# Performance work log

Hardware: AMD Instinct MI355X
Metric: run time of the kernel (lower is better)

The kernel has to match this reference:

```python
import jax, jax.numpy as jnp
import numpy as np

N_NODES = 50000
N_EDGES = 800000
NUM_GRAPHS = 256
BN_EPS = 1e-5


def setup_inputs() -> dict:
    key = jax.random.key(0)
    ks = jax.random.split(key, 16)
    in_dim, hid, out_dim = 64, 128, 1
    s = lambda k, shape, fan: jax.random.normal(k, shape, jnp.float32) / np.sqrt(fan)
    inp = {
        'x': jax.random.normal(ks[0], (N_NODES, in_dim), jnp.float32),
        'edge_index': jax.random.randint(ks[1], (2, N_EDGES), 0, N_NODES, jnp.int64),
        'batch': jnp.sort(jax.random.randint(ks[2], (N_NODES,), 0, NUM_GRAPHS, jnp.int64)),
        # SAGEConv layer 0 (in_dim->hid): Wn aggregated-neighbor weight (with bias), Wr root weight
        'Wn0': s(ks[3], (in_dim, hid), in_dim), 'Wr0': s(ks[4], (in_dim, hid), in_dim), 'b0': jnp.zeros((hid,), jnp.float32),
        'Wn1': s(ks[5], (hid, hid), hid), 'Wr1': s(ks[6], (hid, hid), hid), 'b1': jnp.zeros((hid,), jnp.float32),
        'Wn2': s(ks[7], (hid, hid), hid), 'Wr2': s(ks[8], (hid, hid), hid), 'b2': jnp.zeros((hid,), jnp.float32),
        'gamma': jnp.ones((3, hid), jnp.float32), 'beta': jnp.zeros((3, hid), jnp.float32),
        'fc1_W': s(ks[9], (hid, hid // 2), hid), 'fc1_b': jnp.zeros((hid // 2,), jnp.float32),
        'fc2_W': s(ks[10], (hid // 2, out_dim), hid // 2), 'fc2_b': jnp.zeros((out_dim,), jnp.float32),
    }
    return inp


def _sage_mean(x, src, dst, inv_deg, Wn, Wr, b):
    # mean-aggregate neighbor features then linear: lin_l(mean_j x_j) + lin_r(x_i)
    agg = jax.ops.segment_sum(x[src], dst, num_segments=N_NODES) * inv_deg
    return agg @ Wn + x @ Wr + b


def _bn_relu(h, g, bta):
    mu = jnp.mean(h, axis=0)
    var = jnp.var(h, axis=0)
    return jax.nn.relu((h - mu) * jax.lax.rsqrt(var + BN_EPS) * g + bta)


def reference(x, edge_index, batch, Wn0, Wr0, b0, Wn1, Wr1, b1, Wn2, Wr2, b2,
              gamma, beta, fc1_W, fc1_b, fc2_W, fc2_b):
    src, dst = edge_index[0], edge_index[1]
    deg = jax.ops.segment_sum(jnp.ones((src.shape[0],), x.dtype), dst, num_segments=N_NODES)
    inv_deg = (1.0 / jnp.maximum(deg, 1.0))[:, None]  # [N,1]

    h = _bn_relu(_sage_mean(x, src, dst, inv_deg, Wn0, Wr0, b0), gamma[0], beta[0])
    h = _bn_relu(_sage_mean(h, src, dst, inv_deg, Wn1, Wr1, b1), gamma[1], beta[1])
    h = _bn_relu(_sage_mean(h, src, dst, inv_deg, Wn2, Wr2, b2), gamma[2], beta[2])

    # global mean pool over graphs
    pooled = jax.ops.segment_sum(h, batch, num_segments=NUM_GRAPHS)
    cnt = jax.ops.segment_sum(jnp.ones((h.shape[0],), h.dtype), batch, num_segments=NUM_GRAPHS)
    pooled = pooled / jnp.maximum(cnt, 1.0)[:, None]

    z = jax.nn.relu(pooled @ fc1_W + fc1_b)
    return jax.nn.sigmoid(z @ fc2_W + fc2_b)  # [NUM_GRAPHS, 1]
```

## Files before the change

kernel.cpp:

```cpp
#include <hip/hip_runtime.h>

#define N_NODES 50000
#define N_EDGES 800000
#define NUM_GRAPHS 256
#define HID 128
#define IN_DIM 64
#define BN_EPS 1e-5f
#define SPREAD 16
#define NB 196
#define BUCKET 256
#define SCHUNK 4096
#define NCHUNK 196
#define PX_BLKS 1563
#define W0_BLKS 8
#define W1_BLKS 16

typedef __attribute__((ext_vector_type(8))) short bf16x8;
typedef __attribute__((ext_vector_type(4))) float f32x4;

__device__ __forceinline__ float bf2f(unsigned short u){ union{unsigned i;float f;}c; c.i=((unsigned)u)<<16; return c.f; }
__device__ __forceinline__ float bflo(unsigned w){ union{unsigned i;float f;}c; c.i=w<<16; return c.f; }
__device__ __forceinline__ float bfhi(unsigned w){ union{unsigned i;float f;}c; c.i=w&0xFFFF0000u; return c.f; }
__device__ __forceinline__ unsigned short f2bf(float f){ union{float f;unsigned i;}c; c.f=f; unsigned r=c.i+0x7FFF+((c.i>>16)&1); return (unsigned short)(r>>16); }
__device__ __forceinline__ unsigned fpack(float a, float b){
  union{float f;unsigned i;}ca,cb; ca.f=a; cb.f=b;
  unsigned ra=((ca.i+0x7FFF+((ca.i>>16)&1))>>16)&0xFFFFu;
  unsigned rb=(cb.i+0x7FFF+((cb.i>>16)&1))&0xFFFF0000u;
  return ra|rb;
}
__device__ __forceinline__ void acc8(float* a, uint4 u){
  a[0]+=bflo(u.x); a[1]+=bfhi(u.x); a[2]+=bflo(u.y); a[3]+=bfhi(u.y);
  a[4]+=bflo(u.z); a[5]+=bfhi(u.z); a[6]+=bflo(u.w); a[7]+=bfhi(u.w);
}

__global__ __launch_bounds__(256) void k_hist(const int* __restrict__ dst, int* __restrict__ bcount){
  __shared__ int h[NB];
  int t = threadIdx.x;
  for(int i=t;i<NB;i+=256) h[i]=0;
  __syncthreads();
  int base = blockIdx.x*SCHUNK;
  int n = min(SCHUNK, N_EDGES-base);
  for(int v=t; v<n; v+=256) atomicAdd(&h[dst[base+v]>>8], 1);
  __syncthreads();
  for(int i=t;i<NB;i+=256) if(h[i]) atomicAdd(&bcount[i], h[i]);
}

__global__ __launch_bounds__(256) void k_scatter_pack(const int* __restrict__ src, const int* __restrict__ dst,
      const int* __restrict__ bcount, int* __restrict__ bfill, unsigned* __restrict__ pairs,
      const float* __restrict__ x, unsigned short* __restrict__ H0,
      const float* __restrict__ Wn0, const float* __restrict__ Wr0, unsigned short* __restrict__ Bp0,
      const float* __restrict__ Wn1, const float* __restrict__ Wr1, unsigned short* __restrict__ Bp1,
      const float* __restrict__ Wn2, const float* __restrict__ Wr2, unsigned short* __restrict__ Bp2){
  __shared__ int h[NB], lbase[NB], gbase[NB], cur[NB];
  __shared__ int sc[256];
  __shared__ unsigned staged[SCHUNK];
  int blk = blockIdx.x, t = threadIdx.x;
  if(blk < NCHUNK){
    for(int i=t;i<NB;i+=256) h[i]=0;
    __syncthreads();
    int base = blk*SCHUNK;
    int n = min(SCHUNK, N_EDGES-base);
    for(int v=t; v<n; v+=256) atomicAdd(&h[dst[base+v]>>8], 1);
    __syncthreads();
    int bc = (t<NB)? bcount[t] : 0;
    sc[t]=bc; __syncthreads();
    for(int off=1;off<256;off<<=1){ int u=(t>=off)?sc[t-off]:0; __syncthreads(); sc[t]+=u; __syncthreads(); }
    int bb_t = sc[t]-bc;
    __syncthreads();
    int hv = (t<NB)? h[t] : 0;
    sc[t]=hv; __syncthreads();
    for(int off=1;off<256;off<<=1){ int u=(t>=off)?sc[t-off]:0; __syncthreads(); sc[t]+=u; __syncthreads(); }
    if(t<NB){ lbase[t]=sc[t]-hv; cur[t]=0; if(hv) gbase[t] = bb_t + atomicAdd(&bfill[t], hv); }
    __syncthreads();
    for(int v=t; v<n; v+=256){
      int s = src[base+v], d = dst[base+v];
      int b = d>>8;
      int rr = atomicAdd(&cur[b], 1);
      staged[lbase[b]+rr] = (unsigned)s | ((unsigned)(d&255)<<16) | ((unsigned)b<<24);
    }
    __syncthreads();
    for(int i=t; i<n; i+=256){
      unsigned p = staged[i];
      int b = (int)(p>>24);
      pairs[gbase[b] + (i - lbase[b])] = p;
    }
  } else if(blk < NCHUNK+PX_BLKS){
    int tid = (blk-NCHUNK)*256 + t;
    if(tid < N_NODES*8){
      int row = tid>>3, q = tid&7;
      float4 a = ((const float4*)x)[(size_t)row*16 + q*2];
      float4 b = ((const float4*)x)[(size_t)row*16 + q*2 + 1];
      uint4 o;
      o.x = fpack(a.x,a.y); o.y = fpack(a.z,a.w);
      o.z = fpack(b.x,b.y); o.w = fpack(b.z,b.w);
      ((uint4*)H0)[(size_t)row*8 + q] = o;
    }
  } else {
    const float *Wn, *Wr; unsigned short* Bp; int KH, base;
    if(blk < NCHUNK+PX_BLKS+W0_BLKS){ Wn=Wn0; Wr=Wr0; Bp=Bp0; KH=IN_DIM; base=NCHUNK+PX_BLKS; }
    else if(blk < NCHUNK+PX_BLKS+W0_BLKS+W1_BLKS){ Wn=Wn1; Wr=Wr1; Bp=Bp1; KH=HID; base=NCHUNK+PX_BLKS+W0_BLKS; }
    else { Wn=Wn2; Wr=Wr2; Bp=Bp2; KH=HID; base=NCHUNK+PX_BLKS+W0_BLKS+W1_BLKS; }
    int NKS = (2*KH)/32;
    int id = (blk-base)*256 + t;
    if(id < 8*NKS*64){
      int lane = id & 63;
      int ks = (id>>6) % NKS;
      int nt = (id>>6) / NKS;
      int quad = lane>>4, m = lane&15;
      int c = nt*16 + m;
      unsigned short v[8];
      #pragma unroll
      for(int j=0;j<8;j++){
        int k = ks*32 + quad*8 + j;
        float w = (k < KH) ? Wn[(size_t)k*HID + c] : Wr[(size_t)(k-KH)*HID + c];
        v[j] = f2bf(w);
      }
      uint4 o;
      o.x = ((unsigned)v[1]<<16)|v[0]; o.y = ((unsigned)v[3]<<16)|v[2];
      o.z = ((unsigned)v[5]<<16)|v[4]; o.w = ((unsigned)v[7]<<16)|v[6];
      ((uint4*)Bp)[id] = o;
    }
  }
}

__global__ __launch_bounds__(1024) void k_csr(const unsigned* __restrict__ pairs, const int* __restrict__ bcount,
                int* __restrict__ rowptr, float* __restrict__ invdeg, unsigned short* __restrict__ eidx){
  __shared__ int cnt[BUCKET], cur[BUCKET], sc[BUCKET];
  __shared__ int bb[2];
  int t = threadIdx.x;
  int b = blockIdx.x;
  if(t==0){ bb[0]=0; bb[1]=0; }
  if(t<BUCKET) cnt[t]=0;
  __syncthreads();
  if(t<NB){
    int c = bcount[t];
    if(t<b)  atomicAdd(&bb[0], c);
    if(t<=b) atomicAdd(&bb[1], c);
  }
  __syncthreads();
  int e0 = bb[0], e1 = bb[1];
  int node0 = b*BUCKET;
  for(int i=e0+t; i<e1; i+=1024) atomicAdd(&cnt[(int)((pairs[i]>>16)&0xFF)], 1);
  __syncthreads();
  if(t<BUCKET) sc[t]=cnt[t];
  __syncthreads();
  for(int off=1;off<BUCKET;off<<=1){
    int u=0;
    if(t<BUCKET && t>=off) u=sc[t-off];
    __syncthreads();
    if(t<BUCKET) sc[t]+=u;
    __syncthreads();
  }
  if(t<BUCKET && node0+t < N_NODES){
    int pre = sc[t]-cnt[t] + e0;
    rowptr[node0+t] = pre;
    cur[t] = pre;
    invdeg[node0+t] = 1.0f/(float)max(cnt[t],1);
  }
  if(b==0 && t==0) rowptr[N_NODES] = N_EDGES;
  __syncthreads();
  for(int i=e0+t; i<e1; i+=1024){
    unsigned p = pairs[i];
    int pos = atomicAdd(&cur[(p>>16)&0xFF], 1);
    eidx[pos] = (unsigned short)(p & 0xFFFF);
  }
}

template<int KH>
__global__ __launch_bounds__(256) void k_agg(const unsigned short* __restrict__ H,
                      const unsigned short* __restrict__ eidx, const int* __restrict__ rowptr,
                      const float* __restrict__ invdeg, unsigned short* __restrict__ AGG){
  const int F8  = KH/8;
  const int RPI = 64/F8;
  int wave = threadIdx.x >> 6;
  int lane = threadIdx.x & 63;
  int n = blockIdx.x*4 + wave;
  int b = rowptr[n], e = rowptr[n+1];
  int r = lane / F8, q = lane % F8;
  float acc[8] = {0,0,0,0,0,0,0,0};
  int i = b + r;
  for(; i + 3*RPI < e; i += 4*RPI){
    int s0 = eidx[i], s1 = eidx[i+RPI], s2 = eidx[i+2*RPI], s3 = eidx[i+3*RPI];
    uint4 u0 = *(const uint4*)(H + (size_t)s0*KH + q*8);
    uint4 u1 = *(const uint4*)(H + (size_t)s1*KH + q*8);
    uint4 u2 = *(const uint4*)(H + (size_t)s2*KH + q*8);
    uint4 u3 = *(const uint4*)(H + (size_t)s3*KH + q*8);
    acc8(acc,u0); acc8(acc,u1); acc8(acc,u2); acc8(acc,u3);
  }
  for(; i + RPI < e; i += 2*RPI){
    int s0 = eidx[i], s1 = eidx[i+RPI];
    uint4 u0 = *(const uint4*)(H + (size_t)s0*KH + q*8);
    uint4 u1 = *(const uint4*)(H + (size_t)s1*KH + q*8);
    acc8(acc,u0); acc8(acc,u1);
  }
  for(; i < e; i += RPI){
    int s0 = eidx[i];
    uint4 u0 = *(const uint4*)(H + (size_t)s0*KH + q*8);
    acc8(acc,u0);
  }
  #pragma unroll
  for(int off = F8; off < 64; off <<= 1){
    #pragma unroll
    for(int k=0;k<8;k++) acc[k] += __shfl_xor(acc[k], off, 64);
  }
  if(lane < F8){
    float id = invdeg[n];
    uint4 o;
    o.x = fpack(acc[0]*id, acc[1]*id); o.y = fpack(acc[2]*id, acc[3]*id);
    o.z = fpack(acc[4]*id, acc[5]*id); o.w = fpack(acc[6]*id, acc[7]*id);
    *(uint4*)(AGG + (size_t)n*KH + q*8) = o;
  }
}

template<int KH>
__global__ __launch_bounds__(256) void k_gemm(const unsigned short* __restrict__ AGG,
                     const unsigned short* __restrict__ H,
                     const unsigned short* __restrict__ Bp, const float* __restrict__ bias,
                     unsigned short* __restrict__ raw,
                     float* __restrict__ psum, float* __restrict__ psq){
  const int NKS = (2*KH)/32;
  const int LKS = KH/32;
  int wave = threadIdx.x>>6, lane = threadIdx.x&63;
  int row0w = blockIdx.x*64 + wave*16;
  if(row0w >= N_NODES) return;
  int m = lane&15, quad = lane>>4;
  const unsigned short* Arow = AGG + (size_t)(row0w+m)*KH + quad*8;
  const unsigned short* Hrow = H   + (size_t)(row0w+m)*KH + quad*8;
  f32x4 acc[8];
  #pragma unroll
  for(int nt=0;nt<8;nt++) acc[nt] = (f32x4){0.f,0.f,0.f,0.f};
  #pragma unroll 1
  for(int ks=0; ks<NKS; ks++){
    bf16x8 a = (ks < LKS) ? *(const bf16x8*)(Arow + ks*32)
                          : *(const bf16x8*)(Hrow + (ks-LKS)*32);
    const unsigned short* bp = Bp + ((size_t)ks*64 + lane)*8;
    #pragma unroll
    for(int nt=0;nt<8;nt++){
      bf16x8 b = *(const bf16x8*)(bp + (size_t)nt*NKS*64*8);
      acc[nt] = __builtin_amdgcn_mfma_f32_16x16x32_bf16(a, b, acc[nt], 0, 0, 0);
    }
  }
  int sp = blockIdx.x & (SPREAD-1);
  #pragma unroll
  for(int nt=0;nt<8;nt++){
    int col = nt*16 + m;
    float bv = bias[col];
    float s = 0.f, s2 = 0.f;
    #pragma unroll
    for(int reg=0;reg<4;reg++){
      float v = acc[nt][reg] + bv;
      int row = row0w + quad*4 + reg;
      raw[(size_t)row*HID + col] = f2bf(v);
      s += v; s2 += v*v;
    }
    s  += __shfl_xor(s, 16, 64);  s  += __shfl_xor(s, 32, 64);
    s2 += __shfl_xor(s2, 16, 64); s2 += __shfl_xor(s2, 32, 64);
    if(quad==0){
      atomicAdd(&psum[sp*HID+col], s);
      atomicAdd(&psq [sp*HID+col], s2);
    }
  }
}

__global__ __launch_bounds__(256) void k_transform(const unsigned short* __restrict__ raw,
      const float* __restrict__ psum, const float* __restrict__ psq,
      const float* __restrict__ gamma, const float* __restrict__ beta,
      unsigned short* __restrict__ Hout){
  __shared__ float s_sc[HID], s_sf[HID];
  int t = threadIdx.x;
  if(t < HID){
    float s=0.f, s2=0.f;
    #pragma unroll
    for(int i=0;i<SPREAD;i++){ s += psum[i*HID+t]; s2 += psq[i*HID+t]; }
    float mu  = s  * (1.0f/(float)N_NODES);
    float var = s2 * (1.0f/(float)N_NODES) - mu*mu;
    float rstd = rsqrtf(var + BN_EPS);
    float sc = rstd * gamma[t];
    s_sc[t] = sc; s_sf[t] = beta[t] - mu*sc;
  }
  __syncthreads();
  int tid = blockIdx.x*256 + t;
  if(tid >= N_NODES*16) return;
  int q = tid & 15;
  uint4 u = ((const uint4*)raw)[tid];
  float f0 = fmaxf(fmaf(bflo(u.x), s_sc[q*8+0], s_sf[q*8+0]), 0.f);
  float f1 = fmaxf(fmaf(bfhi(u.x), s_sc[q*8+1], s_sf[q*8+1]), 0.f);
  float f2 = fmaxf(fmaf(bflo(u.y), s_sc[q*8+2], s_sf[q*8+2]), 0.f);
  float f3 = fmaxf(fmaf(bfhi(u.y), s_sc[q*8+3], s_sf[q*8+3]), 0.f);
  float f4 = fmaxf(fmaf(bflo(u.z), s_sc[q*8+4], s_sf[q*8+4]), 0.f);
  float f5 = fmaxf(fmaf(bfhi(u.z), s_sc[q*8+5], s_sf[q*8+5]), 0.f);
  float f6 = fmaxf(fmaf(bflo(u.w), s_sc[q*8+6], s_sf[q*8+6]), 0.f);
  float f7 = fmaxf(fmaf(bfhi(u.w), s_sc[q*8+7], s_sf[q*8+7]), 0.f);
  uint4 o;
  o.x = fpack(f0,f1); o.y = fpack(f2,f3); o.z = fpack(f4,f5); o.w = fpack(f6,f7);
  ((uint4*)Hout)[tid] = o;
}

__global__ __launch_bounds__(128) void k_pool(const unsigned short* __restrict__ raw, const int* __restrict__ batch,
                       const float* __restrict__ psum, const float* __restrict__ psq,
                       const float* __restrict__ gamma, const float* __restrict__ beta,
                       float* __restrict__ pooled, float* __restrict__ cnt){
  const int CH = 32;
  int f = threadIdx.x;
  float s=0.f, s2=0.f;
  #pragma unroll
  for(int i=0;i<SPREAD;i++){ s += psum[i*HID+f]; s2 += psq[i*HID+f]; }
  float mu  = s  * (1.0f/(float)N_NODES);
  float var = s2 * (1.0f/(float)N_NODES) - mu*mu;
  float rstd = rsqrtf(var + BN_EPS);
  float sc = rstd * gamma[f];
  float sf = beta[f] - mu*sc;
  int n0 = blockIdx.x * CH;
  int nEnd = min(n0+CH, N_NODES);
  float acc = 0.f; int curg = -1; int c = 0;
  for(int n=n0;n<nEnd;n++){
    int b = batch[n];
    if(b != curg){
      if(curg >= 0){
        atomicAdd(&pooled[curg*HID+f], acc);
        if(f==0) atomicAdd(&cnt[curg], (float)c);
      }
      acc = 0.f; c = 0; curg = b;
    }
    float v = bf2f(raw[(size_t)n*HID + f]);
    acc += fmaxf(fmaf(v, sc, sf), 0.f);
    c++;
  }
  if(curg >= 0){
    atomicAdd(&pooled[curg*HID+f], acc);
    if(f==0) atomicAdd(&cnt[curg], (float)c);
  }
}

__global__ void k_mlp(const float* __restrict__ pooled, const float* __restrict__ cnt,
                      const float* __restrict__ fc1W, const float* __restrict__ fc1b,
                      const float* __restrict__ fc2W, const float* __restrict__ fc2b,
                      float* __restrict__ out){
  __shared__ float p[HID];
  int g = blockIdx.x; int t = threadIdx.x;
  float ic = 1.0f / fmaxf(cnt[g], 1.0f);
  p[t]      = pooled[g*HID + t]      * ic;
  p[t + 64] = pooled[g*HID + t + 64] * ic;
  __syncthreads();
  float z = fc1b[t];
  #pragma unroll 4
  for(int k=0;k<HID;k++) z += p[k]*fc1W[k*64 + t];
  z = fmaxf(z, 0.f);
  float v = z * fc2W[t];
  #pragma unroll
  for(int off=32; off>0; off>>=1) v += __shfl_down(v, off, 64);
  if(t==0) out[g] = 1.0f/(1.0f + expf(-(v + fc2b[0])));
}

extern "C" void kernel_launch(void* const* d_in, const int* in_sizes, int n_in,
                              void* d_out, int out_size, void* d_ws, size_t ws_size,
                              hipStream_t stream){
  const float* x    = (const float*)d_in[0];
  const int*   ei   = (const int*)d_in[1];
  const int*   batch= (const int*)d_in[2];
  const float* Wn0=(const float*)d_in[3]; const float* Wr0=(const float*)d_in[4]; const float* b0=(const float*)d_in[5];
  const float* Wn1=(const float*)d_in[6]; const float* Wr1=(const float*)d_in[7]; const float* b1=(const float*)d_in[8];
  const float* Wn2=(const float*)d_in[9]; const float* Wr2=(const float*)d_in[10]; const float* b2=(const float*)d_in[11];
  const float* gamma=(const float*)d_in[12]; const float* beta=(const float*)d_in[13];
  const float* fc1W=(const float*)d_in[14]; const float* fc1b=(const float*)d_in[15];
  const float* fc2W=(const float*)d_in[16]; const float* fc2b=(const float*)d_in[17];
  float* out = (float*)d_out;

  char* ws = (char*)d_ws;
  size_t off = 0;
  auto alloc = [&](size_t bytes)->char*{ char* p = ws + off; off += (bytes + 255) & ~(size_t)255; return p; };

  char* zero0   = ws + off;
  int*   bcount = (int*)alloc((size_t)NB*4);
  int*   bfill  = (int*)alloc((size_t)NB*4);
  float* pstats = (float*)alloc((size_t)3*2*SPREAD*HID*4);
  float* pooled = (float*)alloc(((size_t)NUM_GRAPHS*HID + NUM_GRAPHS)*4);
  float* cnt    = pooled + (size_t)NUM_GRAPHS*HID;
  size_t zbytes = (size_t)((ws + off) - zero0);

  unsigned short* H0  = (unsigned short*)alloc((size_t)N_NODES*IN_DIM*2);
  unsigned short* H1  = (unsigned short*)alloc((size_t)N_NODES*HID*2);
  unsigned short* H2  = (unsigned short*)alloc((size_t)N_NODES*HID*2);
  unsigned short* AGG = (unsigned short*)alloc((size_t)N_NODES*HID*2);
  unsigned short* raw = (unsigned short*)alloc((size_t)N_NODES*HID*2);
  unsigned short* Bp0 = (unsigned short*)alloc((size_t)8*4*64*8*2);
  unsigned short* Bp1 = (unsigned short*)alloc((size_t)8*8*64*8*2);
  unsigned short* Bp2 = (unsigned short*)alloc((size_t)8*8*64*8*2);
  float* invdeg = (float*)alloc((size_t)N_NODES*4);
  int* rowptr   = (int*)alloc((size_t)(N_NODES+1)*4);
  unsigned short* eidx = (unsigned short*)alloc((size_t)N_EDGES*2);
  unsigned* pairs = (unsigned*)alloc((size_t)N_EDGES*4);

  auto psumL = [&](int l){ return pstats + (size_t)l*2*SPREAD*HID; };
  auto psqL  = [&](int l){ return pstats + (size_t)l*2*SPREAD*HID + (size_t)SPREAD*HID; };

  const int* src = ei;
  const int* dst = ei + N_EDGES;

  hipMemsetAsync(zero0, 0, zbytes, stream);

  k_hist<<<NCHUNK, 256, 0, stream>>>(dst, bcount);
  k_scatter_pack<<<NCHUNK+PX_BLKS+W0_BLKS+2*W1_BLKS, 256, 0, stream>>>(src, dst, bcount, bfill, pairs,
      x, H0, Wn0, Wr0, Bp0, Wn1, Wr1, Bp1, Wn2, Wr2, Bp2);
  k_csr<<<NB, 1024, 0, stream>>>(pairs, bcount, rowptr, invdeg, eidx);

  const int GEMM_BLKS = (N_NODES + 63)/64;

  k_agg<IN_DIM><<<N_NODES/4, 256, 0, stream>>>(H0, eidx, rowptr, invdeg, AGG);
  k_gemm<IN_DIM><<<GEMM_BLKS, 256, 0, stream>>>(AGG, H0, Bp0, b0, raw, psumL(0), psqL(0));
  k_transform<<<(N_NODES*16)/256, 256, 0, stream>>>(raw, psumL(0), psqL(0), gamma+0*HID, beta+0*HID, H1);
  k_agg<HID><<<N_NODES/4, 256, 0, stream>>>(H1, eidx, rowptr, invdeg, AGG);
  k_gemm<HID><<<GEMM_BLKS, 256, 0, stream>>>(AGG, H1, Bp1, b1, raw, psumL(1), psqL(1));
  k_transform<<<(N_NODES*16)/256, 256, 0, stream>>>(raw, psumL(1), psqL(1), gamma+1*HID, beta+1*HID, H2);
  k_agg<HID><<<N_NODES/4, 256, 0, stream>>>(H2, eidx, rowptr, invdeg, AGG);
  k_gemm<HID><<<GEMM_BLKS, 256, 0, stream>>>(AGG, H2, Bp2, b2, raw, psumL(2), psqL(2));

  k_pool<<<(N_NODES+31)/32, 128, 0, stream>>>(raw, batch, psumL(2), psqL(2), gamma+2*HID, beta+2*HID, pooled, cnt);
  k_mlp<<<NUM_GRAPHS, 64, 0, stream>>>(pooled, cnt, fc1W, fc1b, fc2W, fc2b, out);
}
```

Baseline: 310.9 us.

## Fuse neighbor aggregation into MFMA GEMM and merge pooling with MLP

Each GEMM wave now gathers and mean-aggregates its 16 rows' neighbor features directly into LDS before running the MFMA loop, removing the AGG global buffer round trip and one launch per layer. Pooling is rewritten as one block per graph using per-graph start offsets computed from the sorted batch vector in the pack kernel, fused with the MLP, eliminating atomics and a separate launch. The trade-off is that aggregation parallelism drops: each wave processes 16 nodes serially with 4x fewer blocks, which may reduce latency hiding for the irregular gathers. The per-graph pool relies on batch being sorted, which the input guarantees.

```diff
diff --git a/kernel.cpp b/kernel.cpp
--- a/kernel.cpp
+++ b/kernel.cpp
@@ -14,6 +14,7 @@
 #define PX_BLKS 1563
 #define W0_BLKS 8
 #define W1_BLKS 16
+#define GB_BLKS 196
 
 typedef __attribute__((ext_vector_type(8))) short bf16x8;
 typedef __attribute__((ext_vector_type(4))) float f32x4;
@@ -50,7 +51,8 @@
       const float* __restrict__ x, unsigned short* __restrict__ H0,
       const float* __restrict__ Wn0, const float* __restrict__ Wr0, unsigned short* __restrict__ Bp0,
       const float* __restrict__ Wn1, const float* __restrict__ Wr1, unsigned short* __restrict__ Bp1,
-      const float* __restrict__ Wn2, const float* __restrict__ Wr2, unsigned short* __restrict__ Bp2){
+      const float* __restrict__ Wn2, const float* __restrict__ Wr2, unsigned short* __restrict__ Bp2,
+      const int* __restrict__ batch, int* __restrict__ gstart){
   __shared__ int h[NB], lbase[NB], gbase[NB], cur[NB];
   __shared__ int sc[256];
   __shared__ unsigned staged[SCHUNK];
@@ -95,7 +97,7 @@
       o.z = fpack(b.x,b.y); o.w = fpack(b.z,b.w);
       ((uint4*)H0)[(size_t)row*8 + q] = o;
     }
-  } else {
+  } else if(blk < NCHUNK+PX_BLKS+W0_BLKS+2*W1_BLKS){
     const float *Wn, *Wr; unsigned short* Bp; int KH, base;
     if(blk < NCHUNK+PX_BLKS+W0_BLKS){ Wn=Wn0; Wr=Wr0; Bp=Bp0; KH=IN_DIM; base=NCHUNK+PX_BLKS; }
     else if(blk < NCHUNK+PX_BLKS+W0_BLKS+W1_BLKS){ Wn=Wn1; Wr=Wr1; Bp=Bp1; KH=HID; base=NCHUNK+PX_BLKS+W0_BLKS; }
@@ -120,6 +122,20 @@
       o.z = ((unsigned)v[5]<<16)|v[4]; o.w = ((unsigned)v[7]<<16)|v[6];
       ((uint4*)Bp)[id] = o;
     }
+  } else {
+    int id = (blk - (NCHUNK+PX_BLKS+W0_BLKS+2*W1_BLKS))*256 + t;
+    if(id < N_NODES){
+      int b = batch[id];
+      if(id == 0){
+        for(int g=0; g<=b; g++) gstart[g] = 0;
+      } else {
+        int pv = batch[id-1];
+        if(pv != b) for(int g=pv+1; g<=b; g++) gstart[g] = id;
+      }
+      if(id == N_NODES-1){
+        for(int g=b+1; g<=NUM_GRAPHS; g++) gstart[g] = N_NODES;
+      }
+    }
   }
 }
 
@@ -167,77 +183,77 @@
 }
 
 template<int KH>
-__global__ __launch_bounds__(256) void k_agg(const unsigned short* __restrict__ H,
-                      const unsigned short* __restrict__ eidx, const int* __restrict__ rowptr,
-                      const float* __restrict__ invdeg, unsigned short* __restrict__ AGG){
-  const int F8  = KH/8;
-  const int RPI = 64/F8;
-  int wave = threadIdx.x >> 6;
-  int lane = threadIdx.x & 63;
-  int n = blockIdx.x*4 + wave;
-  int b = rowptr[n], e = rowptr[n+1];
-  int r = lane / F8, q = lane % F8;
-  float acc[8] = {0,0,0,0,0,0,0,0};
-  int i = b + r;
-  for(; i + 3*RPI < e; i += 4*RPI){
-    int s0 = eidx[i], s1 = eidx[i+RPI], s2 = eidx[i+2*RPI], s3 = eidx[i+3*RPI];
-    uint4 u0 = *(const uint4*)(H + (size_t)s0*KH + q*8);
-    uint4 u1 = *(const uint4*)(H + (size_t)s1*KH + q*8);
-    uint4 u2 = *(const uint4*)(H + (size_t)s2*KH + q*8);
-    uint4 u3 = *(const uint4*)(H + (size_t)s3*KH + q*8);
-    acc8(acc,u0); acc8(acc,u1); acc8(acc,u2); acc8(acc,u3);
-  }
-  for(; i + RPI < e; i += 2*RPI){
-    int s0 = eidx[i], s1 = eidx[i+RPI];
-    uint4 u0 = *(const uint4*)(H + (size_t)s0*KH + q*8);
-    uint4 u1 = *(const uint4*)(H + (size_t)s1*KH + q*8);
-    acc8(acc,u0); acc8(acc,u1);
-  }
-  for(; i < e; i += RPI){
-    int s0 = eidx[i];
-    uint4 u0 = *(const uint4*)(H + (size_t)s0*KH + q*8);
-    acc8(acc,u0);
-  }
-  #pragma unroll
-  for(int off = F8; off < 64; off <<= 1){
-    #pragma unroll
-    for(int k=0;k<8;k++) acc[k] += __shfl_xor(acc[k], off, 64);
-  }
-  if(lane < F8){
-    float id = invdeg[n];
-    uint4 o;
-    o.x = fpack(acc[0]*id, acc[1]*id); o.y = fpack(acc[2]*id, acc[3]*id);
-    o.z = fpack(acc[4]*id, acc[5]*id); o.w = fpack(acc[6]*id, acc[7]*id);
-    *(uint4*)(AGG + (size_t)n*KH + q*8) = o;
-  }
-}
-
-template<int KH>
-__global__ __launch_bounds__(256) void k_gemm(const unsigned short* __restrict__ AGG,
-                     const unsigned short* __restrict__ H,
+__global__ __launch_bounds__(256) void k_agg_gemm(const unsigned short* __restrict__ H,
+                     const unsigned short* __restrict__ eidx, const int* __restrict__ rowptr,
+                     const float* __restrict__ invdeg,
                      const unsigned short* __restrict__ Bp, const float* __restrict__ bias,
                      unsigned short* __restrict__ raw,
                      float* __restrict__ psum, float* __restrict__ psq){
   const int NKS = (2*KH)/32;
   const int LKS = KH/32;
+  const int F8  = KH/8;
+  const int RPI = 64/F8;
+  const int LDA = KH + 4;
+  __shared__ unsigned short Alds[64*LDA];
   int wave = threadIdx.x>>6, lane = threadIdx.x&63;
   int row0w = blockIdx.x*64 + wave*16;
   if(row0w >= N_NODES) return;
+
+  int r = lane / F8, q = lane % F8;
+  unsigned short* Aw = Alds + wave*16*LDA;
+  for(int nn=0; nn<16; nn++){
+    int n = row0w + nn;
+    int b = rowptr[n], e = rowptr[n+1];
+    float acc[8] = {0,0,0,0,0,0,0,0};
+    int i = b + r;
+    for(; i + 3*RPI < e; i += 4*RPI){
+      int s0 = eidx[i], s1 = eidx[i+RPI], s2 = eidx[i+2*RPI], s3 = eidx[i+3*RPI];
+      uint4 u0 = *(const uint4*)(H + (size_t)s0*KH + q*8);
+      uint4 u1 = *(const uint4*)(H + (size_t)s1*KH + q*8);
+      uint4 u2 = *(const uint4*)(H + (size_t)s2*KH + q*8);
+      uint4 u3 = *(const uint4*)(H + (size_t)s3*KH + q*8);
+      acc8(acc,u0); acc8(acc,u1); acc8(acc,u2); acc8(acc,u3);
+    }
+    for(; i + RPI < e; i += 2*RPI){
+      int s0 = eidx[i], s1 = eidx[i+RPI];
+      uint4 u0 = *(const uint4*)(H + (size_t)s0*KH + q*8);
+      uint4 u1 = *(const uint4*)(H + (size_t)s1*KH + q*8);
+      acc8(acc,u0); acc8(acc,u1);
+    }
+    for(; i < e; i += RPI){
+      int s0 = eidx[i];
+      uint4 u0 = *(const uint4*)(H + (size_t)s0*KH + q*8);
+      acc8(acc,u0);
+    }
+    #pragma unroll
+    for(int off = F8; off < 64; off <<= 1){
+      #pragma unroll
+      for(int k=0;k<8;k++) acc[k] += __shfl_xor(acc[k], off, 64);
+    }
+    if(lane < F8){
+      float id = invdeg[n];
+      uint4 o;
+      o.x = fpack(acc[0]*id, acc[1]*id); o.y = fpack(acc[2]*id, acc[3]*id);
+      o.z = fpack(acc[4]*id, acc[5]*id); o.w = fpack(acc[6]*id, acc[7]*id);
+      *(uint4*)(Aw + nn*LDA + lane*8) = o;
+    }
+  }
+
   int m = lane&15, quad = lane>>4;
-  const unsigned short* Arow = AGG + (size_t)(row0w+m)*KH + quad*8;
-  const unsigned short* Hrow = H   + (size_t)(row0w+m)*KH + quad*8;
-  f32x4 acc[8];
+  const unsigned short* Arow = Aw + m*LDA + quad*8;
+  const unsigned short* Hrow = H + (size_t)(row0w+m)*KH + quad*8;
+  f32x4 facc[8];
   #pragma unroll
-  for(int nt=0;nt<8;nt++) acc[nt] = (f32x4){0.f,0.f,0.f,0.f};
+  for(int nt=0;nt<8;nt++) facc[nt] = (f32x4){0.f,0.f,0.f,0.f};
   #pragma unroll 1
   for(int ks=0; ks<NKS; ks++){
     bf16x8 a = (ks < LKS) ? *(const bf16x8*)(Arow + ks*32)
-                          : *(const bf16x8*)(Hrow + (ks-LKS)*32);
+                          : *(const bf16x8*)(Hrow + (size_t)(ks-LKS)*32);
     const unsigned short* bp = Bp + ((size_t)ks*64 + lane)*8;
     #pragma unroll
     for(int nt=0;nt<8;nt++){
       bf16x8 b = *(const bf16x8*)(bp + (size_t)nt*NKS*64*8);
-      acc[nt] = __builtin_amdgcn_mfma_f32_16x16x32_bf16(a, b, acc[nt], 0, 0, 0);
+      facc[nt] = __builtin_amdgcn_mfma_f32_16x16x32_bf16(a, b, facc[nt], 0, 0, 0);
     }
   }
   int sp = blockIdx.x & (SPREAD-1);
@@ -248,7 +264,7 @@
     float s = 0.f, s2 = 0.f;
     #pragma unroll
     for(int reg=0;reg<4;reg++){
-      float v = acc[nt][reg] + bv;
+      float v = facc[nt][reg] + bv;
       int row = row0w + quad*4 + reg;
       raw[(size_t)row*HID + col] = f2bf(v);
       s += v; s2 += v*v;
@@ -296,60 +312,63 @@
   ((uint4*)Hout)[tid] = o;
 }
 
-__global__ __launch_bounds__(128) void k_pool(const unsigned short* __restrict__ raw, const int* __restrict__ batch,
-                       const float* __restrict__ psum, const float* __restrict__ psq,
-                       const float* __restrict__ gamma, const float* __restrict__ beta,
-                       float* __restrict__ pooled, float* __restrict__ cnt){
-  const int CH = 32;
-  int f = threadIdx.x;
-  float s=0.f, s2=0.f;
+__global__ __launch_bounds__(256) void k_poolmlp(const unsigned short* __restrict__ raw,
+      const int* __restrict__ gstart,
+      const float* __restrict__ psum, const float* __restrict__ psq,
+      const float* __restrict__ gamma, const float* __restrict__ beta,
+      const float* __restrict__ fc1W, const float* __restrict__ fc1b,
+      const float* __restrict__ fc2W, const float* __restrict__ fc2b,
+      float* __restrict__ out){
+  __shared__ float s_sc[HID], s_sf[HID];
+  __shared__ float red[16][HID];
+  __shared__ float p[HID];
+  int g = blockIdx.x, t = threadIdx.x;
+  if(t < HID){
+    float s=0.f, s2=0.f;
+    #pragma unroll
+    for(int i=0;i<SPREAD;i++){ s += psum[i*HID+t]; s2 += psq[i*HID+t]; }
+    float mu  = s  * (1.0f/(float)N_NODES);
+    float var = s2 * (1.0f/(float)N_NODES) - mu*mu;
+    float rstd = rsqrtf(var + BN_EPS);
+    float sc = rstd * gamma[t];
+    s_sc[t] = sc; s_sf[t] = beta[t] - mu*sc;
+  }
+  __syncthreads();
+  int r0 = gstart[g], r1 = gstart[g+1];
+  int q = t & 15, rr = t >> 4;
+  float acc[8] = {0,0,0,0,0,0,0,0};
+  for(int n = r0 + rr; n < r1; n += 16){
+    uint4 u = ((const uint4*)raw)[(size_t)n*16 + q];
+    acc[0] += fmaxf(fmaf(bflo(u.x), s_sc[q*8+0], s_sf[q*8+0]), 0.f);
+    acc[1] += fmaxf(fmaf(bfhi(u.x), s_sc[q*8+1], s_sf[q*8+1]), 0.f);
+    acc[2] += fmaxf(fmaf(bflo(u.y), s_sc[q*8+2], s_sf[q*8+2]), 0.f);
+    acc[3] += fmaxf(fmaf(bfhi(u.y), s_sc[q*8+3], s_sf[q*8+3]), 0.f);
+    acc[4] += fmaxf(fmaf(bflo(u.z), s_sc[q*8+4], s_sf[q*8+4]), 0.f);
+    acc[5] += fmaxf(fmaf(bfhi(u.z), s_sc[q*8+5], s_sf[q*8+5]), 0.f);
+    acc[6] += fmaxf(fmaf(bflo(u.w), s_sc[q*8+6], s_sf[q*8+6]), 0.f);
+    acc[7] += fmaxf(fmaf(bfhi(u.w), s_sc[q*8+7], s_sf[q*8+7]), 0.f);
+  }
   #pragma unroll
-  for(int i=0;i<SPREAD;i++){ s += psum[i*HID+f]; s2 += psq[i*HID+f]; }
-  float mu  = s  * (1.0f/(float)N_NODES);
-  float var = s2 * (1.0f/(float)N_NODES) - mu*mu;
-  float rstd = rsqrtf(var + BN_EPS);
-  float sc = rstd * gamma[f];
-  float sf = beta[f] - mu*sc;
-  int n0 = blockIdx.x * CH;
-  int nEnd = min(n0+CH, N_NODES);
-  float acc = 0.f; int curg = -1; int c = 0;
-  for(int n=n0;n<nEnd;n++){
-    int b = batch[n];
-    if(b != curg){
-      if(curg >= 0){
-        atomicAdd(&pooled[curg*HID+f], acc);
-        if(f==0) atomicAdd(&cnt[curg], (float)c);
-      }
-      acc = 0.f; c = 0; curg = b;
-    }
-    float v = bf2f(raw[(size_t)n*HID + f]);
-    acc += fmaxf(fmaf(v, sc, sf), 0.f);
-    c++;
-  }
-  if(curg >= 0){
-    atomicAdd(&pooled[curg*HID+f], acc);
-    if(f==0) atomicAdd(&cnt[curg], (float)c);
-  }
-}
-
-__global__ void k_mlp(const float* __restrict__ pooled, const float* __restrict__ cnt,
-                      const float* __restrict__ fc1W, const float* __restrict__ fc1b,
-                      const float* __restrict__ fc2W, const float* __restrict__ fc2b,
-                      float* __restrict__ out){
-  __shared__ float p[HID];
-  int g = blockIdx.x; int t = threadIdx.x;
-  float ic = 1.0f / fmaxf(cnt[g], 1.0f);
-  p[t]      = pooled[g*HID + t]      * ic;
-  p[t + 64] = pooled[g*HID + t + 64] * ic;
-  __syncthreads();
-  float z = fc1b[t];
-  #pragma unroll 4
-  for(int k=0;k<HID;k++) z += p[k]*fc1W[k*64 + t];
-  z = fmaxf(z, 0.f);
-  float v = z * fc2W[t];
-  #pragma unroll
-  for(int off=32; off>0; off>>=1) v += __shfl_down(v, off, 64);
-  if(t==0) out[g] = 1.0f/(1.0f + expf(-(v + fc2b[0])));
+  for(int k=0;k<8;k++) red[rr][q*8+k] = acc[k];
+  __syncthreads();
+  if(t < HID){
+    float s = 0.f;
+    #pragma unroll
+    for(int j=0;j<16;j++) s += red[j][t];
+    float ic = 1.0f / fmaxf((float)(r1 - r0), 1.0f);
+    p[t] = s * ic;
+  }
+  __syncthreads();
+  if(t < 64){
+    float z = fc1b[t];
+    #pragma unroll 4
+    for(int k=0;k<HID;k++) z += p[k]*fc1W[k*64 + t];
+    z = fmaxf(z, 0.f);
+    float v = z * fc2W[t];
+    #pragma unroll
+    for(int off=32; off>0; off>>=1) v += __shfl_down(v, off, 64);
+    if(t==0) out[g] = 1.0f/(1.0f + expf(-(v + fc2b[0])));
+  }
 }
 
 extern "C" void kernel_launch(void* const* d_in, const int* in_sizes, int n_in,
@@ -374,14 +393,11 @@
   int*   bcount = (int*)alloc((size_t)NB*4);
   int*   bfill  = (int*)alloc((size_t)NB*4);
   float* pstats = (float*)alloc((size_t)3*2*SPREAD*HID*4);
-  float* pooled = (float*)alloc(((size_t)NUM_GRAPHS*HID + NUM_GRAPHS)*4);
-  float* cnt    = pooled + (size_t)NUM_GRAPHS*HID;
   size_t zbytes = (size_t)((ws + off) - zero0);
 
   unsigned short* H0  = (unsigned short*)alloc((size_t)N_NODES*IN_DIM*2);
   unsigned short* H1  = (unsigned short*)alloc((size_t)N_NODES*HID*2);
   unsigned short* H2  = (unsigned short*)alloc((size_t)N_NODES*HID*2);
-  unsigned short* AGG = (unsigned short*)alloc((size_t)N_NODES*HID*2);
   unsigned short* raw = (unsigned short*)alloc((size_t)N_NODES*HID*2);
   unsigned short* Bp0 = (unsigned short*)alloc((size_t)8*4*64*8*2);
   unsigned short* Bp1 = (unsigned short*)alloc((size_t)8*8*64*8*2);
@@ -390,6 +406,7 @@
   int* rowptr   = (int*)alloc((size_t)(N_NODES+1)*4);
   unsigned short* eidx = (unsigned short*)alloc((size_t)N_EDGES*2);
   unsigned* pairs = (unsigned*)alloc((size_t)N_EDGES*4);
+  int* gstart   = (int*)alloc((size_t)(NUM_GRAPHS+1)*4);
 
   auto psumL = [&](int l){ return pstats + (size_t)l*2*SPREAD*HID; };
   auto psqL  = [&](int l){ return pstats + (size_t)l*2*SPREAD*HID + (size_t)SPREAD*HID; };
@@ -400,21 +417,18 @@
   hipMemsetAsync(zero0, 0, zbytes, stream);
 
   k_hist<<<NCHUNK, 256, 0, stream>>>(dst, bcount);
-  k_scatter_pack<<<NCHUNK+PX_BLKS+W0_BLKS+2*W1_BLKS, 256, 0, stream>>>(src, dst, bcount, bfill, pairs,
-      x, H0, Wn0, Wr0, Bp0, Wn1, Wr1, Bp1, Wn2, Wr2, Bp2);
+  k_scatter_pack<<<NCHUNK+PX_BLKS+W0_BLKS+2*W1_BLKS+GB_BLKS, 256, 0, stream>>>(src, dst, bcount, bfill, pairs,
+      x, H0, Wn0, Wr0, Bp0, Wn1, Wr1, Bp1, Wn2, Wr2, Bp2, batch, gstart);
   k_csr<<<NB, 1024, 0, stream>>>(pairs, bcount, rowptr, invdeg, eidx);
 
   const int GEMM_BLKS = (N_NODES + 63)/64;
 
-  k_agg<IN_DIM><<<N_NODES/4, 256, 0, stream>>>(H0, eidx, rowptr, invdeg, AGG);
-  k_gemm<IN_DIM><<<GEMM_BLKS, 256, 0, stream>>>(AGG, H0, Bp0, b0, raw, psumL(0), psqL(0));
+  k_agg_gemm<IN_DIM><<<GEMM_BLKS, 256, 0, stream>>>(H0, eidx, rowptr, invdeg, Bp0, b0, raw, psumL(0), psqL(0));
   k_transform<<<(N_NODES*16)/256, 256, 0, stream>>>(raw, psumL(0), psqL(0), gamma+0*HID, beta+0*HID, H1);
-  k_agg<HID><<<N_NODES/4, 256, 0, stream>>>(H1, eidx, rowptr, invdeg, AGG);
-  k_gemm<HID><<<GEMM_BLKS, 256, 0, stream>>>(AGG, H1, Bp1, b1, raw, psumL(1), psqL(1));
+  k_agg_gemm<HID><<<GEMM_BLKS, 256, 0, stream>>>(H1, eidx, rowptr, invdeg, Bp1, b1, raw, psumL(1), psqL(1));
   k_transform<<<(N_NODES*16)/256, 256, 0, stream>>>(raw, psumL(1), psqL(1), gamma+1*HID, beta+1*HID, H2);
-  k_agg<HID><<<N_NODES/4, 256, 0, stream>>>(H2, eidx, rowptr, invdeg, AGG);
-  k_gemm<HID><<<GEMM_BLKS, 256, 0, stream>>>(AGG, H2, Bp2, b2, raw, psumL(2), psqL(2));
-
-  k_pool<<<(N_NODES+31)/32, 128, 0, stream>>>(raw, batch, psumL(2), psqL(2), gamma+2*HID, beta+2*HID, pooled, cnt);
-  k_mlp<<<NUM_GRAPHS, 64, 0, stream>>>(pooled, cnt, fc1W, fc1b, fc2W, fc2b, out);
-}
+  k_agg_gemm<HID><<<GEMM_BLKS, 256, 0, stream>>>(H2, eidx, rowptr, invdeg, Bp2, b2, raw, psumL(2), psqL(2));
+
+  k_poolmlp<<<NUM_GRAPHS, 256, 0, stream>>>(raw, gstart, psumL(2), psqL(2), gamma+2*HID, beta+2*HID,
+      fc1W, fc1b, fc2W, fc2b, out);
+}
```

After: 330.9 us. 1.06x slower.
